# Optimization experiments

Measured on AMD Instinct MI355X. Metric: run time of the kernel, lower is better.

Reference implementation:

```python
import jax, jax.numpy as jnp
import numpy as np

# Instant-NGP multi-resolution hash grid constants (match init_kwargs)
L = 16            # num_levels
F = 2             # level_dim (features per level)
LOG2T = 19
T = 1 << LOG2T    # hashmap entries per level
BASE = 16.0       # base_resolution
SCALE = 1.3819061 # per_level_scale
HIDDEN = 64
N = 500_000
P1 = jnp.uint32(2654435761)  # NGP spatial hash primes (prime for dim0 is 1)
P2 = jnp.uint32(805459861)
# 8 corner offsets of the voxel, [8,3]
OFFS = jnp.array([[i, j, k] for i in (0, 1) for j in (0, 1) for k in (0, 1)], dtype=jnp.float32)


def hash_encode(x, table):
    # x: [N,3] in [0,1];  table: [L,T,F]
    res = jnp.floor(BASE * SCALE ** jnp.arange(L, dtype=jnp.float32))   # [L]
    pos = x[None] * (res[:, None, None] - 1.0)                          # [L,N,3]
    p0 = jnp.floor(pos)
    f = pos - p0                                                        # trilinear fracs [L,N,3]
    pi = p0.astype(jnp.uint32)                                          # [L,N,3]
    offs_u = OFFS.astype(jnp.uint32)                                    # [8,3]
    cx = pi[..., 0:1] + offs_u[None, None, :, 0]                        # [L,N,8]
    cy = pi[..., 1:2] + offs_u[None, None, :, 1]
    cz = pi[..., 2:3] + offs_u[None, None, :, 2]
    idx = (cx ^ (cy * P1) ^ (cz * P2)) & jnp.uint32(T - 1)              # [L,N,8] hashed table index
    feats = jax.vmap(lambda tab, i: tab[i])(table, idx)                 # per-level gather -> [L,N,8,F]
    # trilinear weights: prod over dims of (f if corner bit set else 1-f)
    w = jnp.prod(jnp.where(OFFS[None, None] > 0.5, f[:, :, None, :], 1.0 - f[:, :, None, :]), axis=-1)  # [L,N,8]
    out = jnp.einsum('lnc,lncf->lnf', w, feats)                         # [L,N,F]
    return out.transpose(1, 0, 2).reshape(x.shape[0], L * F)           # [N, L*F]


def setup_inputs() -> dict:
    key = jax.random.key(0)
    k = jax.random.split(key, 8)
    x = jax.random.uniform(k[0], (N, 3), dtype=jnp.float32)
    # NGP-style small uniform init for the hash tables
    table = jax.random.normal(k[1], (L, T, F), dtype=jnp.float32) * 1e-4
    feat_dim = L * F
    w1 = jax.random.normal(k[2], (feat_dim, HIDDEN), dtype=jnp.float32) / np.sqrt(feat_dim)
    b1 = jnp.zeros((HIDDEN,), jnp.float32)
    w2 = jax.random.normal(k[3], (HIDDEN, HIDDEN), dtype=jnp.float32) / np.sqrt(HIDDEN)
    b2 = jnp.zeros((HIDDEN,), jnp.float32)
    w3 = jax.random.normal(k[4], (HIDDEN, 3), dtype=jnp.float32) / np.sqrt(HIDDEN)
    b3 = jnp.zeros((3,), jnp.float32)
    return {"x": x, "table": table, "w1": w1, "b1": b1, "w2": w2, "b2": b2, "w3": w3, "b3": b3}


def reference(x, table, w1, b1, w2, b2, w3, b3):
    feat = hash_encode(x, table)                         # [N, 32]
    h = jax.nn.relu(feat @ w1 + b1)
    h = jax.nn.relu(h @ w2 + b2)
    rgb = jax.nn.sigmoid(h @ w3 + b3)                    # [N, 3]
    return rgb
```

## Files before the change

kernel.cpp:

```cpp
#include <hip/hip_runtime.h>
#include <hip/hip_fp16.h>
#include <math.h>


constexpr int      LVLS   = 16;
constexpr uint32_t TSIZE  = 1u << 19;
constexpr uint32_t TMASK  = TSIZE - 1u;
constexpr uint32_t PRIME1 = 2654435761u;
constexpr uint32_t PRIME2 = 805459861u;

struct ResArr { float v[LVLS]; };

typedef __attribute__((ext_vector_type(8))) short short8v;
typedef __attribute__((ext_vector_type(4))) float float4v;

__device__ inline ushort f2bf(float f) {
    uint u = __float_as_uint(f);
    u += 0x7fffu + ((u >> 16) & 1u);
    return (ushort)(u >> 16);
}

__global__ __launch_bounds__(256)
void ingp_prep(const float* __restrict__ w1, const float* __restrict__ w2,
               const float* __restrict__ w3,
               ushort* __restrict__ w1t, ushort* __restrict__ w2t,
               ushort* __restrict__ w3t)
{
    const int t = blockIdx.x * 256 + threadIdx.x;
    if (t < 2048) {
        const int nn = t >> 5, k = t & 31;
        w1t[t] = f2bf(w1[k * 64 + nn]);
    } else if (t < 2048 + 4096) {
        const int q = t - 2048;
        const int nn = q >> 6, k = q & 63;
        w2t[q] = f2bf(w2[k * 64 + nn]);
    } else if (t < 2048 + 4096 + 1024) {
        const int q = t - 6144;
        const int nn = q >> 6, k = q & 63;
        w3t[q] = (nn < 3) ? f2bf(w3[k * 3 + nn]) : (ushort)0;
    }
}

__global__ __launch_bounds__(256, 8)
void ingp_encode(const float* __restrict__ x,
                 const float* __restrict__ table,
                 uint* __restrict__ feat, int n, ResArr res)
{
    const int i = blockIdx.x * 256 + threadIdx.x;
    const int l = blockIdx.y;
    if (i >= n) return;

    const float xx = x[3 * i + 0];
    const float xy = x[3 * i + 1];
    const float xz = x[3 * i + 2];

    const float rm1 = res.v[l];
    const float px = xx * rm1, py = xy * rm1, pz = xz * rm1;
    const float fpx = floorf(px), fpy = floorf(py), fpz = floorf(pz);
    const float fx = px - fpx, fy = py - fpy, fz = pz - fpz;
    const uint32_t ix = (uint32_t)fpx;
    const uint32_t iy = (uint32_t)fpy;
    const uint32_t iz = (uint32_t)fpz;
    const uint32_t hy0 = iy * PRIME1, hy1 = (iy + 1u) * PRIME1;
    const uint32_t hz0 = iz * PRIME2, hz1 = (iz + 1u) * PRIME2;
    const float* tl = table + (size_t)l * (size_t)TSIZE * 2u;

    uint32_t idx0[4], idx1[4];
    #pragma unroll
    for (int p = 0; p < 4; ++p) {
        const uint32_t bj = (p >> 1) & 1, bk = p & 1;
        const uint32_t hyz = (bj ? hy1 : hy0) ^ (bk ? hz1 : hz0);
        idx0[p] = (ix ^ hyz) & TMASK;
        idx1[p] = ((ix + 1u) ^ hyz) & TMASK;
    }

    float2 c0[4], c1[4];
    if ((ix & 1u) == 0u) {
        #pragma unroll
        for (int p = 0; p < 4; ++p) {
            const uint32_t base = idx0[p] & ~1u;
            const float4 q = *reinterpret_cast<const float4*>(tl + (size_t)base * 2u);
            if (idx0[p] & 1u) {
                c0[p] = make_float2(q.z, q.w);
                c1[p] = make_float2(q.x, q.y);
            } else {
                c0[p] = make_float2(q.x, q.y);
                c1[p] = make_float2(q.z, q.w);
            }
        }
    } else {
        #pragma unroll
        for (int p = 0; p < 4; ++p) {
            c0[p] = *reinterpret_cast<const float2*>(tl + (size_t)idx0[p] * 2u);
            c1[p] = *reinterpret_cast<const float2*>(tl + (size_t)idx1[p] * 2u);
        }
    }

    const float gx0 = 1.f - fx, gx1 = fx;
    float a0 = 0.f, a1 = 0.f;
    #pragma unroll
    for (int p = 0; p < 4; ++p) {
        const int bj = (p >> 1) & 1, bk = p & 1;
        const float wyz = (bj ? fy : 1.f - fy) * (bk ? fz : 1.f - fz);
        const float w0 = wyz * gx0, w1 = wyz * gx1;
        a0 = fmaf(w0, c0[p].x, a0);
        a1 = fmaf(w0, c0[p].y, a1);
        a0 = fmaf(w1, c1[p].x, a0);
        a1 = fmaf(w1, c1[p].y, a1);
    }
    feat[(size_t)l * n + i] = (uint)f2bf(a0) | ((uint)f2bf(a1) << 16);
}

__global__ __launch_bounds__(256)
void ingp_mlp_mfma(const uint* __restrict__ feat,
                   const ushort* __restrict__ w1t,
                   const ushort* __restrict__ w2t,
                   const ushort* __restrict__ w3t,
                   const float* __restrict__ b1,
                   const float* __restrict__ b2,
                   const float* __restrict__ b3,
                   float* __restrict__ out, int n)
{
    __shared__ ushort s_h[4][64][72];
    const int tid = threadIdx.x;
    const int wv = tid >> 6;
    const int ln = tid & 63;
    const int lm = ln & 15;
    const int lk = ln >> 4;
    const int base = blockIdx.x * 256 + wv * 64;

    short8v a1[4];
    #pragma unroll
    for (int mt = 0; mt < 4; ++mt) {
        int pt = base + mt * 16 + lm;
        pt = pt < n ? pt : (n - 1);
        union { uint u[4]; short8v v; } c;
        #pragma unroll
        for (int j = 0; j < 4; ++j)
            c.u[j] = feat[(size_t)(lk * 4 + j) * (size_t)n + pt];
        a1[mt] = c.v;
    }

    float4v acc[4][4];
    #pragma unroll
    for (int nt = 0; nt < 4; ++nt) {
        const float bv = b1[nt * 16 + lm];
        #pragma unroll
        for (int mt = 0; mt < 4; ++mt)
            acc[mt][nt] = (float4v){bv, bv, bv, bv};
    }
    #pragma unroll
    for (int nt = 0; nt < 4; ++nt) {
        const short8v bfr = *(const short8v*)(w1t + (nt * 16 + lm) * 32 + lk * 8);
        #pragma unroll
        for (int mt = 0; mt < 4; ++mt)
            acc[mt][nt] = __builtin_amdgcn_mfma_f32_16x16x32_bf16(
                a1[mt], bfr, acc[mt][nt], 0, 0, 0);
    }
    #pragma unroll
    for (int mt = 0; mt < 4; ++mt)
        #pragma unroll
        for (int nt = 0; nt < 4; ++nt)
            #pragma unroll
            for (int r = 0; r < 4; ++r)
                s_h[wv][mt * 16 + lk * 4 + r][nt * 16 + lm] =
                    f2bf(fmaxf(acc[mt][nt][r], 0.f));
    __syncthreads();

    float4v acc2[4][4];
    #pragma unroll
    for (int nt = 0; nt < 4; ++nt) {
        const float bv = b2[nt * 16 + lm];
        #pragma unroll
        for (int mt = 0; mt < 4; ++mt)
            acc2[mt][nt] = (float4v){bv, bv, bv, bv};
    }
    #pragma unroll
    for (int ks = 0; ks < 2; ++ks) {
        short8v a2[4];
        #pragma unroll
        for (int mt = 0; mt < 4; ++mt)
            a2[mt] = *(const short8v*)&s_h[wv][mt * 16 + lm][ks * 32 + lk * 8];
        #pragma unroll
        for (int nt = 0; nt < 4; ++nt) {
            const short8v bfr =
                *(const short8v*)(w2t + (nt * 16 + lm) * 64 + ks * 32 + lk * 8);
            #pragma unroll
            for (int mt = 0; mt < 4; ++mt)
                acc2[mt][nt] = __builtin_amdgcn_mfma_f32_16x16x32_bf16(
                    a2[mt], bfr, acc2[mt][nt], 0, 0, 0);
        }
    }
    __syncthreads();
    #pragma unroll
    for (int mt = 0; mt < 4; ++mt)
        #pragma unroll
        for (int nt = 0; nt < 4; ++nt)
            #pragma unroll
            for (int r = 0; r < 4; ++r)
                s_h[wv][mt * 16 + lk * 4 + r][nt * 16 + lm] =
                    f2bf(fmaxf(acc2[mt][nt][r], 0.f));
    __syncthreads();

    float4v acc3[4];
    const float bv3 = (lm < 3) ? b3[lm] : 0.f;
    #pragma unroll
    for (int mt = 0; mt < 4; ++mt)
        acc3[mt] = (float4v){bv3, bv3, bv3, bv3};
    #pragma unroll
    for (int ks = 0; ks < 2; ++ks) {
        const short8v bfr = *(const short8v*)(w3t + lm * 64 + ks * 32 + lk * 8);
        #pragma unroll
        for (int mt = 0; mt < 4; ++mt) {
            const short8v a3 =
                *(const short8v*)&s_h[wv][mt * 16 + lm][ks * 32 + lk * 8];
            acc3[mt] = __builtin_amdgcn_mfma_f32_16x16x32_bf16(
                a3, bfr, acc3[mt], 0, 0, 0);
        }
    }
    if (lm < 3) {
        #pragma unroll
        for (int mt = 0; mt < 4; ++mt)
            #pragma unroll
            for (int r = 0; r < 4; ++r) {
                const int pt = base + mt * 16 + lk * 4 + r;
                if (pt < n)
                    out[pt * 3 + lm] = 1.f / (1.f + __expf(-acc3[mt][r]));
            }
    }
}

__global__ __launch_bounds__(256)
void ingp_mlp(const __half2* __restrict__ feat16,
              const float* __restrict__ w1, const float* __restrict__ b1,
              const float* __restrict__ w2, const float* __restrict__ b2,
              const float* __restrict__ w3, const float* __restrict__ b3,
              float* __restrict__ out, int n)
{
    __shared__ float s_w1[32 * 64];
    __shared__ float s_w2[64 * 64];
    __shared__ float s_w3[64 * 3];
    __shared__ float s_b1[64];
    __shared__ float s_b2[64];
    __shared__ float s_b3[3];
    for (int t = threadIdx.x; t < 32 * 64; t += 256) s_w1[t] = w1[t];
    for (int t = threadIdx.x; t < 64 * 64; t += 256) s_w2[t] = w2[t];
    for (int t = threadIdx.x; t < 64 * 3;  t += 256) s_w3[t] = w3[t];
    if (threadIdx.x < 64) { s_b1[threadIdx.x] = b1[threadIdx.x]; s_b2[threadIdx.x] = b2[threadIdx.x]; }
    if (threadIdx.x < 3) s_b3[threadIdx.x] = b3[threadIdx.x];
    __syncthreads();
    const int i = blockIdx.x * 256 + threadIdx.x;
    if (i >= n) return;
    float feat[32];
    #pragma unroll
    for (int l = 0; l < LVLS; ++l) {
        const float2 f = __half22float2(feat16[(size_t)l * n + i]);
        feat[2 * l + 0] = f.x;
        feat[2 * l + 1] = f.y;
    }
    float h1[64];
    #pragma unroll
    for (int j = 0; j < 64; ++j) h1[j] = s_b1[j];
    #pragma unroll
    for (int k = 0; k < 32; ++k) {
        const float fv = feat[k];
        #pragma unroll
        for (int j = 0; j < 64; ++j) h1[j] = fmaf(fv, s_w1[k * 64 + j], h1[j]);
    }
    #pragma unroll
    for (int j = 0; j < 64; ++j) h1[j] = fmaxf(h1[j], 0.f);
    float h2[64];
    #pragma unroll
    for (int j = 0; j < 64; ++j) h2[j] = s_b2[j];
    #pragma unroll
    for (int k = 0; k < 64; ++k) {
        const float hv = h1[k];
        #pragma unroll
        for (int j = 0; j < 64; ++j) h2[j] = fmaf(hv, s_w2[k * 64 + j], h2[j]);
    }
    #pragma unroll
    for (int j = 0; j < 64; ++j) h2[j] = fmaxf(h2[j], 0.f);
    float o0 = s_b3[0], o1 = s_b3[1], o2 = s_b3[2];
    #pragma unroll
    for (int j = 0; j < 64; ++j) {
        const float hv = h2[j];
        o0 = fmaf(hv, s_w3[j * 3 + 0], o0);
        o1 = fmaf(hv, s_w3[j * 3 + 1], o1);
        o2 = fmaf(hv, s_w3[j * 3 + 2], o2);
    }
    out[3 * i + 0] = 1.f / (1.f + __expf(-o0));
    out[3 * i + 1] = 1.f / (1.f + __expf(-o1));
    out[3 * i + 2] = 1.f / (1.f + __expf(-o2));
}

__global__ __launch_bounds__(256, 8)
void ingp_encode_h2(const float* __restrict__ x,
                    const float* __restrict__ table,
                    __half2* __restrict__ feat16, int n, ResArr res)
{
    const int i = blockIdx.x * 256 + threadIdx.x;
    const int l = blockIdx.y;
    if (i >= n) return;
    const float xx = x[3 * i + 0], xy = x[3 * i + 1], xz = x[3 * i + 2];
    const float rm1 = res.v[l];
    const float px = xx * rm1, py = xy * rm1, pz = xz * rm1;
    const float fpx = floorf(px), fpy = floorf(py), fpz = floorf(pz);
    const float fx = px - fpx, fy = py - fpy, fz = pz - fpz;
    const uint32_t ix = (uint32_t)fpx, iy = (uint32_t)fpy, iz = (uint32_t)fpz;
    const uint32_t hy0 = iy * PRIME1, hy1 = (iy + 1u) * PRIME1;
    const uint32_t hz0 = iz * PRIME2, hz1 = (iz + 1u) * PRIME2;
    const float* tl = table + (size_t)l * (size_t)TSIZE * 2u;
    float a0 = 0.f, a1 = 0.f;
    #pragma unroll
    for (int c = 0; c < 8; ++c) {
        const int bi = (c >> 2) & 1, bj = (c >> 1) & 1, bk = c & 1;
        const uint32_t h = ((ix + (uint32_t)bi) ^ (bj ? hy1 : hy0) ^ (bk ? hz1 : hz0)) & TMASK;
        const float2 tv = *reinterpret_cast<const float2*>(tl + (size_t)h * 2u);
        const float w = (bi ? fx : 1.f - fx) * (bj ? fy : 1.f - fy) * (bk ? fz : 1.f - fz);
        a0 = fmaf(w, tv.x, a0);
        a1 = fmaf(w, tv.y, a1);
    }
    feat16[(size_t)l * n + i] = __floats2half2_rn(a0, a1);
}

extern "C" void kernel_launch(void* const* d_in, const int* in_sizes, int n_in,
                              void* d_out, int out_size, void* d_ws, size_t ws_size,
                              hipStream_t stream)
{
    const float* x     = (const float*)d_in[0];
    const float* table = (const float*)d_in[1];
    const float* w1    = (const float*)d_in[2];
    const float* b1    = (const float*)d_in[3];
    const float* w2    = (const float*)d_in[4];
    const float* b2    = (const float*)d_in[5];
    const float* w3    = (const float*)d_in[6];
    const float* b3    = (const float*)d_in[7];
    float* out = (float*)d_out;

    const int n = in_sizes[0] / 3;

    ResArr res;
    const double S = (double)1.3819061f;
    double p = 1.0;
    for (int l = 0; l < LVLS; ++l) {
        res.v[l] = (float)floor(16.0 * p) - 1.0f;
        p *= S;
    }

    const int gb = (n + 255) / 256;
    const size_t feat_bytes = (size_t)LVLS * (size_t)n * 4u;
    const size_t need_mfma  = 16384 + feat_bytes;

    if (ws_size >= need_mfma) {
        ushort* w1t = (ushort*)d_ws;
        ushort* w2t = w1t + 2048;
        ushort* w3t = w2t + 4096;
        uint*   feat = (uint*)((char*)d_ws + 16384);
        ingp_prep<<<28, 256, 0, stream>>>(w1, w2, w3, w1t, w2t, w3t);
        dim3 gridA(gb, LVLS);
        ingp_encode<<<gridA, 256, 0, stream>>>(x, table, feat, n, res);
        ingp_mlp_mfma<<<gb, 256, 0, stream>>>(feat, w1t, w2t, w3t,
                                              b1, b2, b3, out, n);
    } else {
        dim3 gridA(gb, LVLS);
        ingp_encode_h2<<<gridA, 256, 0, stream>>>(x, table, (__half2*)d_ws, n, res);
        ingp_mlp<<<gb, 256, 0, stream>>>((const __half2*)d_ws,
                                         w1, b1, w2, b2, w3, b3, out, n);
    }
}
```

Before: 201.8 us.

## Convert hash table to fp16 each call and gather 16-byte blocks

Adds a conversion kernel that runs every call, turning the fp32 hash table into packed half2 entries and padding x to float4. The encode kernel then gathers both x-neighbour corners from one 16-byte load whenever they share an aligned group of four entries. The goal is to halve the bytes moved by the random gathers and improve how often corners share a cache line. The trade-offs are an extra pass over the whole 64 MB table (read 64 MB, write 32 MB) on every call and reduced precision of the table values.

```diff
diff --git a/kernel.cpp b/kernel.cpp
--- a/kernel.cpp
+++ b/kernel.cpp
@@ -18,6 +18,36 @@
     uint u = __float_as_uint(f);
     u += 0x7fffu + ((u >> 16) & 1u);
     return (ushort)(u >> 16);
+}
+
+__device__ inline float2 h2f(uint u) {
+    __half2 h = *reinterpret_cast<__half2*>(&u);
+    return __half22float2(h);
+}
+
+__device__ inline uint pick4(const uint4& b, uint j) {
+    const uint lo = (j & 1u) ? b.y : b.x;
+    const uint hi = (j & 1u) ? b.w : b.z;
+    return (j & 2u) ? hi : lo;
+}
+
+__global__ __launch_bounds__(256)
+void ingp_conv(const float* __restrict__ table, uint* __restrict__ tab16,
+               const float* __restrict__ x, float4* __restrict__ x4, int n)
+{
+    const int t = blockIdx.x * 256 + threadIdx.x;
+    const int HALF = LVLS * (int)TSIZE / 2;
+    if (t < HALF) {
+        const float4 v = *reinterpret_cast<const float4*>(table + (size_t)t * 4u);
+        __half2 ha = __floats2half2_rn(v.x, v.y);
+        __half2 hb = __floats2half2_rn(v.z, v.w);
+        uint2 o;
+        o.x = *reinterpret_cast<uint*>(&ha);
+        o.y = *reinterpret_cast<uint*>(&hb);
+        *reinterpret_cast<uint2*>(tab16 + (size_t)t * 2u) = o;
+    }
+    if (t < n)
+        x4[t] = make_float4(x[3 * t + 0], x[3 * t + 1], x[3 * t + 2], 0.f);
 }
 
 __global__ __launch_bounds__(256)
@@ -42,20 +72,17 @@
 }
 
 __global__ __launch_bounds__(256, 8)
-void ingp_encode(const float* __restrict__ x,
-                 const float* __restrict__ table,
-                 uint* __restrict__ feat, int n, ResArr res)
+void ingp_encode_f16(const float4* __restrict__ x4,
+                     const uint* __restrict__ tab16,
+                     uint* __restrict__ feat, int n, ResArr res)
 {
     const int i = blockIdx.x * 256 + threadIdx.x;
     const int l = blockIdx.y;
     if (i >= n) return;
 
-    const float xx = x[3 * i + 0];
-    const float xy = x[3 * i + 1];
-    const float xz = x[3 * i + 2];
-
+    const float4 xp = x4[i];
     const float rm1 = res.v[l];
-    const float px = xx * rm1, py = xy * rm1, pz = xz * rm1;
+    const float px = xp.x * rm1, py = xp.y * rm1, pz = xp.z * rm1;
     const float fpx = floorf(px), fpy = floorf(py), fpz = floorf(pz);
     const float fx = px - fpx, fy = py - fpy, fz = pz - fpz;
     const uint32_t ix = (uint32_t)fpx;
@@ -63,6 +90,67 @@
     const uint32_t iz = (uint32_t)fpz;
     const uint32_t hy0 = iy * PRIME1, hy1 = (iy + 1u) * PRIME1;
     const uint32_t hz0 = iz * PRIME2, hz1 = (iz + 1u) * PRIME2;
+    const uint* tl = tab16 + (size_t)l * (size_t)TSIZE;
+
+    uint32_t h0[4], h1[4];
+    #pragma unroll
+    for (int p = 0; p < 4; ++p) {
+        const uint32_t bj = (p >> 1) & 1, bk = p & 1;
+        const uint32_t hyz = (bj ? hy1 : hy0) ^ (bk ? hz1 : hz0);
+        h0[p] = (ix ^ hyz) & TMASK;
+        h1[p] = ((ix + 1u) ^ hyz) & TMASK;
+    }
+
+    uint e0[4], e1[4];
+    if ((ix & 3u) != 3u) {
+        #pragma unroll
+        for (int p = 0; p < 4; ++p) {
+            const uint32_t base = h0[p] & ~3u;
+            const uint4 blk = *reinterpret_cast<const uint4*>(tl + base);
+            e0[p] = pick4(blk, h0[p] & 3u);
+            e1[p] = pick4(blk, h1[p] & 3u);
+        }
+    } else {
+        #pragma unroll
+        for (int p = 0; p < 4; ++p) {
+            e0[p] = tl[h0[p]];
+            e1[p] = tl[h1[p]];
+        }
+    }
+
+    const float gx0 = 1.f - fx, gx1 = fx;
+    float a0 = 0.f, a1 = 0.f;
+    #pragma unroll
+    for (int p = 0; p < 4; ++p) {
+        const int bj = (p >> 1) & 1, bk = p & 1;
+        const float wyz = (bj ? fy : 1.f - fy) * (bk ? fz : 1.f - fz);
+        const float w0 = wyz * gx0, w1 = wyz * gx1;
+        const float2 c0 = h2f(e0[p]);
+        const float2 c1 = h2f(e1[p]);
+        a0 = fmaf(w0, c0.x, a0);
+        a1 = fmaf(w0, c0.y, a1);
+        a0 = fmaf(w1, c1.x, a0);
+        a1 = fmaf(w1, c1.y, a1);
+    }
+    feat[(size_t)l * n + i] = (uint)f2bf(a0) | ((uint)f2bf(a1) << 16);
+}
+
+__global__ __launch_bounds__(256, 8)
+void ingp_encode(const float* __restrict__ x,
+                 const float* __restrict__ table,
+                 uint* __restrict__ feat, int n, ResArr res)
+{
+    const int i = blockIdx.x * 256 + threadIdx.x;
+    const int l = blockIdx.y;
+    if (i >= n) return;
+    const float xx = x[3 * i + 0], xy = x[3 * i + 1], xz = x[3 * i + 2];
+    const float rm1 = res.v[l];
+    const float px = xx * rm1, py = xy * rm1, pz = xz * rm1;
+    const float fpx = floorf(px), fpy = floorf(py), fpz = floorf(pz);
+    const float fx = px - fpx, fy = py - fpy, fz = pz - fpz;
+    const uint32_t ix = (uint32_t)fpx, iy = (uint32_t)fpy, iz = (uint32_t)fpz;
+    const uint32_t hy0 = iy * PRIME1, hy1 = (iy + 1u) * PRIME1;
+    const uint32_t hz0 = iz * PRIME2, hz1 = (iz + 1u) * PRIME2;
     const float* tl = table + (size_t)l * (size_t)TSIZE * 2u;
 
     uint32_t idx0[4], idx1[4];
@@ -73,20 +161,14 @@
         idx0[p] = (ix ^ hyz) & TMASK;
         idx1[p] = ((ix + 1u) ^ hyz) & TMASK;
     }
-
     float2 c0[4], c1[4];
     if ((ix & 1u) == 0u) {
         #pragma unroll
         for (int p = 0; p < 4; ++p) {
             const uint32_t base = idx0[p] & ~1u;
             const float4 q = *reinterpret_cast<const float4*>(tl + (size_t)base * 2u);
-            if (idx0[p] & 1u) {
-                c0[p] = make_float2(q.z, q.w);
-                c1[p] = make_float2(q.x, q.y);
-            } else {
-                c0[p] = make_float2(q.x, q.y);
-                c1[p] = make_float2(q.z, q.w);
-            }
+            if (idx0[p] & 1u) { c0[p] = make_float2(q.z, q.w); c1[p] = make_float2(q.x, q.y); }
+            else              { c0[p] = make_float2(q.x, q.y); c1[p] = make_float2(q.z, q.w); }
         }
     } else {
         #pragma unroll
@@ -95,7 +177,6 @@
             c1[p] = *reinterpret_cast<const float2*>(tl + (size_t)idx1[p] * 2u);
         }
     }
-
     const float gx0 = 1.f - fx, gx1 = fx;
     float a0 = 0.f, a1 = 0.f;
     #pragma unroll
@@ -349,9 +430,32 @@
 
     const int gb = (n + 255) / 256;
     const size_t feat_bytes = (size_t)LVLS * (size_t)n * 4u;
-    const size_t need_mfma  = 16384 + feat_bytes;
-
-    if (ws_size >= need_mfma) {
+    const size_t tab16_bytes = (size_t)LVLS * (size_t)TSIZE * 4u;
+    const size_t x4_bytes   = (size_t)n * 16u;
+
+    const size_t off_tab16 = 16384;
+    const size_t off_feat  = off_tab16 + tab16_bytes;
+    const size_t off_x4    = off_feat + feat_bytes;
+    const size_t need_full = off_x4 + x4_bytes;
+    const size_t need_mid  = 16384 + feat_bytes;
+
+    if (ws_size >= need_full) {
+        ushort* w1t  = (ushort*)d_ws;
+        ushort* w2t  = w1t + 2048;
+        ushort* w3t  = w2t + 4096;
+        uint*   tab16 = (uint*)((char*)d_ws + off_tab16);
+        uint*   feat  = (uint*)((char*)d_ws + off_feat);
+        float4* x4    = (float4*)((char*)d_ws + off_x4);
+
+        const int conv_threads = LVLS * (int)TSIZE / 2;
+        ingp_conv<<<(conv_threads + 255) / 256, 256, 0, stream>>>(
+            table, tab16, x, x4, n);
+        ingp_prep<<<28, 256, 0, stream>>>(w1, w2, w3, w1t, w2t, w3t);
+        dim3 gridA(gb, LVLS);
+        ingp_encode_f16<<<gridA, 256, 0, stream>>>(x4, tab16, feat, n, res);
+        ingp_mlp_mfma<<<gb, 256, 0, stream>>>(feat, w1t, w2t, w3t,
+                                              b1, b2, b3, out, n);
+    } else if (ws_size >= need_mid) {
         ushort* w1t = (ushort*)d_ws;
         ushort* w2t = w1t + 2048;
         ushort* w3t = w2t + 4096;
```

Result: faster. 179.5 us (-11.1%).
